# Kernel optimization log

Measured on AMD Instinct MI355X. Metric: run time of the kernel, lower is better.

## Reference

```python
import jax, jax.numpy as jnp
import numpy as np

B, L, C, P, H, DK, MRD = 16, 1024, 512, 64, 8, 64, 7
STD = 0.02


def _layernorm(x, g, b):
    mu = x.mean(-1, keepdims=True)
    var = ((x - mu) ** 2).mean(-1, keepdims=True)
    return (x - mu) / jnp.sqrt(var + 1e-5) * g + b


def _rel_pos_table(L, m):
    i = jnp.arange(L)
    d = jnp.abs(i[:, None] - i[None, :]).astype(jnp.float32)
    d = jnp.where(d > m, m + jnp.log2(jnp.maximum(d - m, 1.0)), d)
    return jnp.clip(d, 0, 2 * m).astype(jnp.int32)  # (L, L) in [0, 2m]


def setup_inputs() -> dict:
    key = jax.random.key(0)
    ks = jax.random.split(key, 16)
    inp = {
        'qx': jax.random.normal(ks[0], (B, L, C), jnp.float32),
        'kx': jax.random.normal(ks[1], (B, L, C), jnp.float32),
        'vx': jax.random.normal(ks[2], (B, L, C), jnp.float32),
        'maskPAD': jnp.ones((B, L, L), jnp.int32),
        'Wp': jax.random.normal(ks[3], (C, P)) * STD,
        'bp': jnp.zeros((P,)),
        'WQ': jax.random.normal(ks[4], (C, H * DK)) * STD,
        'bQ': jnp.zeros((H * DK,)),
        'WK': jax.random.normal(ks[5], (C, H * DK)) * STD,
        'bK': jnp.zeros((H * DK,)),
        'WV': jax.random.normal(ks[6], (C, H * DK)) * STD,
        'bV': jnp.zeros((H * DK,)),
        'WO': jax.random.normal(ks[7], (H * DK, C)) * STD,
        'bO': jnp.zeros((C,)),
        'embK': jax.random.normal(ks[8], (2 * MRD + 1, H)) * STD,
        'embB': jax.random.normal(ks[9], (2 * MRD + 1, H)) * STD,
        'ln1_g': jnp.ones((C,)), 'ln1_b': jnp.zeros((C,)),
        'ln2_g': jnp.ones((C,)), 'ln2_b': jnp.zeros((C,)),
        'W1': jax.random.normal(ks[10], (C, 4 * C)) * STD,
        'b1': jnp.zeros((4 * C,)),
        'W2': jax.random.normal(ks[11], (4 * C, C)) * STD,
        'b2': jnp.zeros((C,)),
    }
    return inp


def reference(qx, kx, vx, maskPAD, Wp, bp, WQ, bQ, WK, bK, WV, bV, WO, bO,
              embK, embB, ln1_g, ln1_b, ln2_g, ln2_b, W1, b1, W2, b2):
    B_, L_, C_ = qx.shape
    P_ = Wp.shape[1]
    H_ = embK.shape[1]
    DK_ = WV.shape[1] // H_
    m = (embK.shape[0] - 1) // 2

    # pseudo-token attention pooling
    pScore = vx @ Wp + bp                                   # (B, L, P)
    pad = (maskPAD[:, 0] == 0)                              # (B, L)
    pScore = jnp.where(pad[:, :, None], -2.0 ** 15, pScore)
    pAlpha = jax.nn.softmax(pScore, axis=1)                 # softmax over L
    kxp = jnp.einsum('blp,blc->bpc', pAlpha, kx)            # (B, P, C)
    vxp = jnp.einsum('blp,blc->bpc', pAlpha, vx)
    pA = jax.lax.stop_gradient(pAlpha)                      # .detach()

    # multi-head attention vs pseudo tokens
    q = (qx @ WQ + bQ).reshape(B_, L_, H_, DK_).transpose(0, 2, 1, 3)   # (B,H,L,dk)
    k = (kxp @ WK + bK).reshape(B_, P_, H_, DK_).transpose(0, 2, 1, 3)  # (B,H,P,dk)
    v = (vxp @ WV + bV).reshape(B_, P_, H_, DK_).transpose(0, 2, 1, 3)
    scores = jnp.einsum('bhld,bhpd->bhlp', q, k) / np.sqrt(DK_).astype(np.float32)

    # relative position multiplicative/additive bias, pooled through pA
    tab = _rel_pos_table(L_, m)                             # (L, L)
    Krel = embK[tab].transpose(2, 0, 1)                     # (H, L, L)
    brel = embB[tab].transpose(2, 0, 1)
    Kb = jnp.einsum('hlm,bmp->bhlp', Krel, pA)
    bb = jnp.einsum('hlm,bmp->bhlp', brel, pA)
    scores = scores * Kb + bb

    alpha = jax.nn.softmax(scores, axis=3)
    z = jnp.einsum('bhlp,bhpd->bhld', alpha, v)
    z = z.transpose(0, 2, 1, 3).reshape(B_, L_, H_ * DK_)
    z = z @ WO + bO

    # FFN block (residuals against vx, post-LN)
    z1 = _layernorm(vx + z, ln1_g, ln1_b)
    ffn = jax.nn.gelu(z1 @ W1 + b1, approximate=False) @ W2 + b2
    x = _layernorm(z1 + ffn, ln2_g, ln2_b)
    return x
```

## Files before the change

### kernel.cpp

```cpp
#include <hip/hip_runtime.h>
#include <hip/hip_bf16.h>

#define BI   16
#define LSEQ 1024
#define CDIM 512
#define PDIM 64
#define HH   8
#define DKK  64

typedef __hip_bfloat16 bf16;
typedef unsigned short u16;
typedef __attribute__((ext_vector_type(8))) short bf16x8;
typedef __attribute__((ext_vector_type(4))) float f32x4;

__constant__ int c_dlo[15] = {0,1,2,3,4,5,6,7, 9,11,15,23,39, 71,135};
__constant__ int c_dhi[15] = {0,1,2,3,4,5,6,8,10,14,22,38,70,134,1023};

__device__ __forceinline__ float b2f(u16 u) {
    union { unsigned int i; float f; } c; c.i = ((unsigned int)u) << 16; return c.f;
}
__device__ __forceinline__ u16 f2bu(float v) {
    bf16 h = __float2bfloat16(v);
    return *(u16*)&h;
}
__device__ __forceinline__ float ldDyn(const void* p, size_t i, int f) {
    return f ? ((const float*)p)[i] : b2f(((const u16*)p)[i]);
}
__device__ __forceinline__ void ld4Dyn(const void* p, size_t i, int f, float* o) {
    if (f) { float4 v = *(const float4*)((const float*)p + i);
             o[0]=v.x; o[1]=v.y; o[2]=v.z; o[3]=v.w; }
    else   { ushort4 u = *(const ushort4*)((const u16*)p + i);
             o[0]=b2f(u.x); o[1]=b2f(u.y); o[2]=b2f(u.z); o[3]=b2f(u.w); }
}

__device__ __forceinline__ void gll16(const u16* g, u16* l) {
    __builtin_amdgcn_global_load_lds(
        (const __attribute__((address_space(1))) unsigned int*)g,
        (__attribute__((address_space(3))) unsigned int*)l,
        16, 0, 0);
}

__device__ __forceinline__ float wsum(float v) {
    #pragma unroll
    for (int o = 32; o; o >>= 1) v += __shfl_xor(v, o, 64);
    return v;
}
__device__ __forceinline__ float wmax(float v) {
    #pragma unroll
    for (int o = 32; o; o >>= 1) v = fmaxf(v, __shfl_xor(v, o, 64));
    return v;
}

__global__ void k_detect(const unsigned int* __restrict__ qw, int* __restrict__ flag) {
    __shared__ int cnt;
    if (threadIdx.x == 0) cnt = 0;
    __syncthreads();
    int local = 0;
    for (int i = threadIdx.x; i < 4096; i += 256) {
        float fv = b2f((u16)(qw[i] & 0xFFFFu));
        float af = fabsf(fv);
        if (fv == 0.0f || (af >= 0.0009765625f && af <= 32.0f)) local++;
    }
    atomicAdd(&cnt, local);
    __syncthreads();
    if (threadIdx.x == 0) flag[0] = (cnt >= 2048) ? 0 : 1;
}

__global__ __launch_bounds__(256) void k_cvt2(
    const void* __restrict__ s0, u16* __restrict__ d0,
    const void* __restrict__ s1, u16* __restrict__ d1,
    const int* __restrict__ flag, int n)
{
    const int fA = flag[0];
    const void* src = blockIdx.y ? s1 : s0;
    u16* dst = blockIdx.y ? d1 : d0;
    int i = (blockIdx.x * 256 + threadIdx.x) * 4;
    if (i >= n) return;
    float t[4]; ld4Dyn(src, i, fA, t);
    ushort4 o; o.x = f2bu(t[0]); o.y = f2bu(t[1]); o.z = f2bu(t[2]); o.w = f2bu(t[3]);
    *(ushort4*)(dst + i) = o;
}

__device__ __forceinline__ void transp_core(
    const void* W, u16* WT, int fd, int Kd, int Nd, int bx, int by)
{
    __shared__ u16 t[32][33];
    const int tx = threadIdx.x & 31, ty = threadIdx.x >> 5;
    #pragma unroll
    for (int r = 0; r < 32; r += 8) {
        int k = by * 32 + ty + r, n = bx * 32 + tx;
        t[ty + r][tx] = f2bu(ldDyn(W, (size_t)k * Nd + n, fd));
    }
    __syncthreads();
    #pragma unroll
    for (int r = 0; r < 32; r += 8) {
        int n = bx * 32 + ty + r, k = by * 32 + tx;
        WT[(size_t)n * Kd + k] = t[tx][ty + r];
    }
}

__global__ __launch_bounds__(256) void k_transp(
    const void* __restrict__ W, u16* __restrict__ WT, const int* __restrict__ flag,
    int Kd, int Nd)
{
    transp_core(W, WT, flag[0], Kd, Nd, blockIdx.x, blockIdx.y);
}

__global__ __launch_bounds__(256) void k_transp4(
    const void* __restrict__ W0, u16* __restrict__ T0,
    const void* __restrict__ W1, u16* __restrict__ T1,
    const void* __restrict__ W2, u16* __restrict__ T2,
    const void* __restrict__ W3, u16* __restrict__ T3,
    const int* __restrict__ flag)
{
    const void* W; u16* T;
    switch (blockIdx.z) {
        case 0: W = W0; T = T0; break;
        case 1: W = W1; T = T1; break;
        case 2: W = W2; T = T2; break;
        default: W = W3; T = T3; break;
    }
    transp_core(W, T, flag[0], 512, 512, blockIdx.x, blockIdx.y);
}

__global__ __launch_bounds__(256) void k_transpcv(
    const void* __restrict__ kx, const u16* __restrict__ vxb,
    u16* __restrict__ kxT, u16* __restrict__ vxT, const int* __restrict__ flag)
{
    const int t = blockIdx.z >> 4;
    const int b = blockIdx.z & 15;
    const int l0 = blockIdx.x * 64, c0 = blockIdx.y * 32;
    __shared__ u16 s[32][72];
    const int tid = threadIdx.x;
    if (t == 0) {
        const int fd = flag[0];
        #pragma unroll
        for (int p = 0; p < 2; ++p) {
            int l = (tid >> 3) + p * 32, c4 = (tid & 7) * 4;
            float v[4];
            ld4Dyn(kx, ((size_t)b * LSEQ + l0 + l) * CDIM + c0 + c4, fd, v);
            #pragma unroll
            for (int k = 0; k < 4; ++k) s[c4 + k][l] = f2bu(v[k]);
        }
    } else {
        #pragma unroll
        for (int p = 0; p < 2; ++p) {
            int l = (tid >> 3) + p * 32, c4 = (tid & 7) * 4;
            ushort4 u = *(const ushort4*)&vxb[((size_t)b * LSEQ + l0 + l) * CDIM + c0 + c4];
            s[c4 + 0][l] = u.x; s[c4 + 1][l] = u.y;
            s[c4 + 2][l] = u.z; s[c4 + 3][l] = u.w;
        }
    }
    __syncthreads();
    u16* dst = t ? vxT : kxT;
    #pragma unroll
    for (int p = 0; p < 2; ++p) {
        int c = (tid >> 4) + p * 16, l4 = (tid & 15) * 4;
        *(ushort4*)&dst[((size_t)b * CDIM + c0 + c) * LSEQ + l0 + l4] =
            *(const ushort4*)&s[c][l4];
    }
}

__device__ __forceinline__ void gemm_core(
    u16 (*As)[32], u16 (*Bs)[32],
    const u16* A, const u16* BT, const void* bias, const u16* res, void* Cc, int fd,
    int K, int lda, int ldbt, int ldc, size_t bOff, int mode, int outBf, int perm,
    int m0, int n0)
{
    const int tid = threadIdx.x;
    const int wave = tid >> 6, lane = tid & 63;
    const int q = lane >> 4, l16 = lane & 15;
    const int wm = (wave >> 1) * 64, wn = (wave & 1) * 64;
    const int srow = wave * 16 + (lane >> 2);
    const int scol = ((lane & 3) ^ ((lane >> 3) & 3)) * 8;
    const int rchk = (l16 >> 1) & 3;
    const int nt = K >> 5;

    f32x4 acc[4][4];
    #pragma unroll
    for (int i = 0; i < 4; ++i)
        #pragma unroll
        for (int j = 0; j < 4; ++j) acc[i][j] = (f32x4){0.f, 0.f, 0.f, 0.f};

    auto stage = [&](int t, int buf) {
        const int o = buf * 128;
        #pragma unroll
        for (int pass = 0; pass < 2; ++pass) {
            int row = pass * 64 + srow;
            gll16(A + (size_t)(m0 + row) * lda + t * 32 + scol,
                  &As[o + pass * 64 + wave * 16][0]);
            gll16(BT + (size_t)(n0 + row) * ldbt + t * 32 + scol,
                  &Bs[o + pass * 64 + wave * 16][0]);
        }
    };

    stage(0, 0);

    for (int t = 0; t < nt; ++t) {
        if (t + 1 < nt) {
            stage(t + 1, (t + 1) & 1);
            asm volatile("s_waitcnt vmcnt(4)" ::: "memory");
        } else {
            asm volatile("s_waitcnt vmcnt(0)" ::: "memory");
        }
        __builtin_amdgcn_sched_barrier(0);
        __builtin_amdgcn_s_barrier();

        const int cb = (t & 1) * 128;
        bf16x8 af[4], bfr[4];
        #pragma unroll
        for (int i = 0; i < 4; ++i)
            af[i] = *(const bf16x8*)&As[cb + wm + i * 16 + l16][(q ^ rchk) * 8];
        #pragma unroll
        for (int j = 0; j < 4; ++j)
            bfr[j] = *(const bf16x8*)&Bs[cb + wn + j * 16 + l16][(q ^ rchk) * 8];
        #pragma unroll
        for (int i = 0; i < 4; ++i)
            #pragma unroll
            for (int j = 0; j < 4; ++j)
                acc[i][j] = __builtin_amdgcn_mfma_f32_16x16x32_bf16(af[i], bfr[j], acc[i][j], 0, 0, 0);

        if (t + 1 < nt) {
            asm volatile("s_waitcnt lgkmcnt(0)" ::: "memory");
            __builtin_amdgcn_sched_barrier(0);
            __builtin_amdgcn_s_barrier();
        }
    }

    #pragma unroll
    for (int i = 0; i < 4; ++i) {
        int row = m0 + wm + i * 16 + q * 4;
        #pragma unroll
        for (int j = 0; j < 4; ++j) {
            int col = n0 + wn + j * 16 + l16;
            #pragma unroll
            for (int r = 0; r < 4; ++r) {
                float v = acc[i][j][r];
                int m = row + r;
                if (mode == 2) {
                    v += ldDyn(bias, bOff + col, fd) + b2f(res[(size_t)m * ldc + col]);
                    ((float*)Cc)[(size_t)m * ldc + col] = v;
                } else {
                    v += ldDyn(bias, bOff + col, fd);
                    if (mode == 1) v = 0.5f * v * (1.0f + erff(v * 0.70710678118654752f));
                    size_t idx = perm ? (size_t)((m >> 6) << 15) + ((size_t)col << 6) + (m & 63)
                                      : (size_t)m * ldc + col;
                    if (outBf) ((u16*)Cc)[idx] = f2bu(v);
                    else       ((float*)Cc)[idx] = v;
                }
            }
        }
    }
}

__global__ __launch_bounds__(256) void gemm_mfma(
    const u16* __restrict__ A, const u16* __restrict__ BT, const void* __restrict__ bias,
    const u16* __restrict__ res, void* __restrict__ Cc, const int* __restrict__ flag,
    int K, int lda, int ldbt, int ldc, size_t bOff, int mode, int outBf, int perm)
{
    __shared__ u16 As[256][32];
    __shared__ u16 Bs[256][32];
    const int lin = blockIdx.y * gridDim.x + blockIdx.x;
    const int chunk = (gridDim.x * gridDim.y) >> 3;
    const int wg = (lin & 7) * chunk + (lin >> 3);
    const int bx = wg % gridDim.x, by = wg / gridDim.x;
    gemm_core(As, Bs, A, BT, bias, res, Cc, flag[0], K, lda, ldbt, ldc, bOff,
              mode, outBf, perm, by * 128, bx * 128);
}

__global__ __launch_bounds__(256) void gemm_kv(
    const u16* __restrict__ A0, const u16* __restrict__ A1,
    const u16* __restrict__ BT0, const u16* __restrict__ BT1,
    const void* __restrict__ b0, const void* __restrict__ b1,
    void* __restrict__ C0, void* __restrict__ C1, const int* __restrict__ flag)
{
    __shared__ u16 As[256][32];
    __shared__ u16 Bs[256][32];
    const int z = blockIdx.z;
    gemm_core(As, Bs, z ? A1 : A0, z ? BT1 : BT0, z ? b1 : b0, nullptr,
              z ? C1 : C0, flag[0],
              CDIM, CDIM, CDIM, CDIM, 0, 0, 1, z ? 1 : 0,
              blockIdx.y * 128, blockIdx.x * 128);
}

__global__ __launch_bounds__(256) void gemm_pool(
    const u16* __restrict__ pAT, const u16* __restrict__ kxT,
    const u16* __restrict__ vxT, u16* __restrict__ kvxb)
{
    __shared__ u16 As[128][32];
    __shared__ u16 Bs[256][32];
    const int b = blockIdx.y;
    const int n0 = blockIdx.x * 128;
    const u16* Ag = pAT + (size_t)b * (PDIM * LSEQ);
    const u16* Bg = (blockIdx.z ? vxT : kxT) + (size_t)b * (CDIM * LSEQ);
    u16* Cg = kvxb + (size_t)blockIdx.z * 524288 + (size_t)b * (PDIM * CDIM);

    const int tid = threadIdx.x;
    const int wave = tid >> 6, lane = tid & 63;
    const int q = lane >> 4, l16 = lane & 15;
    const int wm = (wave >> 1) * 32, wn = (wave & 1) * 64;
    const int srow = lane >> 2, scol = (lane & 3) * 8;

    f32x4 acc[2][4];
    #pragma unroll
    for (int i = 0; i < 2; ++i)
        #pragma unroll
        for (int j = 0; j < 4; ++j) acc[i][j] = (f32x4){0.f, 0.f, 0.f, 0.f};

    gll16(Ag + (size_t)(wave * 16 + srow) * LSEQ + scol, &As[wave * 16][0]);
    #pragma unroll
    for (int pass = 0; pass < 2; ++pass)
        gll16(Bg + (size_t)(n0 + wave * 32 + pass * 16 + srow) * LSEQ + scol,
              &Bs[wave * 32 + pass * 16][0]);
    __syncthreads();

    int cur = 0;
    for (int k0 = 0; k0 < LSEQ; k0 += 32) {
        if (k0 + 32 < LSEQ) {
            const int na = (cur ^ 1) * 64, nb = (cur ^ 1) * 128;
            gll16(Ag + (size_t)(wave * 16 + srow) * LSEQ + (k0 + 32) + scol,
                  &As[na + wave * 16][0]);
            #pragma unroll
            for (int pass = 0; pass < 2; ++pass)
                gll16(Bg + (size_t)(n0 + wave * 32 + pass * 16 + srow) * LSEQ + (k0 + 32) + scol,
                      &Bs[nb + wave * 32 + pass * 16][0]);
        }
        const int ca = cur * 64, cb = cur * 128;
        bf16x8 af[2], bfr[4];
        #pragma unroll
        for (int i = 0; i < 2; ++i) af[i] = *(const bf16x8*)&As[ca + wm + i * 16 + l16][q * 8];
        #pragma unroll
        for (int j = 0; j < 4; ++j) bfr[j] = *(const bf16x8*)&Bs[cb + wn + j * 16 + l16][q * 8];
        #pragma unroll
        for (int i = 0; i < 2; ++i)
            #pragma unroll
            for (int j = 0; j < 4; ++j)
                acc[i][j] = __builtin_amdgcn_mfma_f32_16x16x32_bf16(af[i], bfr[j], acc[i][j], 0, 0, 0);
        __syncthreads();
        cur ^= 1;
    }

    #pragma unroll
    for (int i = 0; i < 2; ++i) {
        int row = wm + i * 16 + q * 4;
        #pragma unroll
        for (int j = 0; j < 4; ++j) {
            int col = n0 + wn + j * 16 + l16;
            #pragma unroll
            for (int r = 0; r < 4; ++r)
                Cg[(size_t)(row + r) * CDIM + col] = f2bu(acc[i][j][r]);
        }
    }
}

__global__ __launch_bounds__(256) void gemm_mfma64(
    const u16* __restrict__ A, const u16* __restrict__ BT, const void* __restrict__ bias,
    float* __restrict__ Cc, const int* __restrict__ flag,
    int K, int lda, int ldbt)
{
    const int fd = flag[0];
    __shared__ u16 As[256][32];
    __shared__ u16 Bs[128][32];
    const int m0 = blockIdx.y * 128;
    const int tid = threadIdx.x;
    const int wave = tid >> 6, lane = tid & 63;
    const int q = lane >> 4, l16 = lane & 15;
    const int wm = wave * 32;
    const int srow = wave * 16 + (lane >> 2);
    const int scol = (lane & 3) * 8;

    f32x4 acc[2][4];
    #pragma unroll
    for (int i = 0; i < 2; ++i)
        #pragma unroll
        for (int j = 0; j < 4; ++j) acc[i][j] = (f32x4){0.f, 0.f, 0.f, 0.f};

    #pragma unroll
    for (int pass = 0; pass < 2; ++pass) {
        int row = pass * 64 + srow;
        gll16(A + (size_t)(m0 + row) * lda + scol, &As[pass * 64 + wave * 16][0]);
    }
    gll16(BT + (size_t)srow * ldbt + scol, &Bs[wave * 16][0]);
    __syncthreads();

    int cur = 0;
    for (int k0 = 0; k0 < K; k0 += 32) {
        if (k0 + 32 < K) {
            const int na = (cur ^ 1) * 128, nb = (cur ^ 1) * 64;
            #pragma unroll
            for (int pass = 0; pass < 2; ++pass) {
                int row = pass * 64 + srow;
                gll16(A + (size_t)(m0 + row) * lda + (k0 + 32) + scol,
                      &As[na + pass * 64 + wave * 16][0]);
            }
            gll16(BT + (size_t)srow * ldbt + (k0 + 32) + scol, &Bs[nb + wave * 16][0]);
        }
        const int ca = cur * 128, cb = cur * 64;
        bf16x8 af[2], bfr[4];
        #pragma unroll
        for (int i = 0; i < 2; ++i) af[i] = *(const bf16x8*)&As[ca + wm + i * 16 + l16][q * 8];
        #pragma unroll
        for (int j = 0; j < 4; ++j) bfr[j] = *(const bf16x8*)&Bs[cb + j * 16 + l16][q * 8];
        #pragma unroll
        for (int i = 0; i < 2; ++i)
            #pragma unroll
            for (int j = 0; j < 4; ++j)
                acc[i][j] = __builtin_amdgcn_mfma_f32_16x16x32_bf16(af[i], bfr[j], acc[i][j], 0, 0, 0);
        __syncthreads();
        cur ^= 1;
    }

    #pragma unroll
    for (int i = 0; i < 2; ++i) {
        int row = m0 + wm + i * 16 + q * 4;
        #pragma unroll
        for (int j = 0; j < 4; ++j) {
            int col = j * 16 + l16;
            #pragma unroll
            for (int r = 0; r < 4; ++r)
                Cc[(size_t)(row + r) * 64 + col] = acc[i][j][r] + ldDyn(bias, col, fd);
        }
    }
}

__global__ __launch_bounds__(256) void gemm_att(
    const u16* __restrict__ Abase, const u16* __restrict__ Bbase,
    void* __restrict__ outp, int mode)
{
    __shared__ u16 Aq[2][128][32];
    __shared__ u16 Bk[2][64][32];
    const int bh = blockIdx.y;
    const int b = bh >> 3, h = bh & 7;
    const int m0 = blockIdx.x * 128;
    const int tid = threadIdx.x;
    const int wave = tid >> 6, lane = tid & 63;
    const int q = lane >> 4, l16 = lane & 15;

    const u16* Ag; const u16* Bg; int lda, ldb;
    if (mode == 0) {
        Ag = Abase + ((size_t)b * LSEQ + m0) * CDIM + h * 64;  lda = CDIM;
        Bg = Bbase + (size_t)b * 32768 + h * 64;               ldb = CDIM;
    } else {
        Ag = Abase + ((size_t)bh * LSEQ + m0) * 64;            lda = 64;
        Bg = Bbase + (size_t)b * 32768 + (size_t)h * 64 * 64;  ldb = 64;
    }

    const int srow = lane >> 2;
    const int scol = (lane & 3) * 8;
    #pragma unroll
    for (int half = 0; half < 2; ++half) {
        #pragma unroll
        for (int pass = 0; pass < 2; ++pass) {
            int row = pass * 64 + wave * 16 + srow;
            gll16(Ag + (size_t)row * lda + half * 32 + scol,
                  &Aq[half][pass * 64 + wave * 16][0]);
        }
        gll16(Bg + (size_t)(wave * 16 + srow) * ldb + half * 32 + scol,
              &Bk[half][wave * 16][0]);
    }
    __syncthreads();

    f32x4 acc[2][4];
    #pragma unroll
    for (int i = 0; i < 2; ++i)
        #pragma unroll
        for (int j = 0; j < 4; ++j) acc[i][j] = (f32x4){0.f, 0.f, 0.f, 0.f};

    #pragma unroll
    for (int kk = 0; kk < 2; ++kk) {
        bf16x8 af[2], bfr[4];
        #pragma unroll
        for (int i = 0; i < 2; ++i)
            af[i] = *(const bf16x8*)&Aq[kk][wave * 32 + i * 16 + l16][q * 8];
        #pragma unroll
        for (int j = 0; j < 4; ++j)
            bfr[j] = *(const bf16x8*)&Bk[kk][j * 16 + l16][q * 8];
        #pragma unroll
        for (int i = 0; i < 2; ++i)
            #pragma unroll
            for (int j = 0; j < 4; ++j)
                acc[i][j] = __builtin_amdgcn_mfma_f32_16x16x32_bf16(af[i], bfr[j], acc[i][j], 0, 0, 0);
    }

    #pragma unroll
    for (int i = 0; i < 2; ++i) {
        int row = m0 + wave * 32 + i * 16 + q * 4;
        #pragma unroll
        for (int j = 0; j < 4; ++j) {
            int col = j * 16 + l16;
            #pragma unroll
            for (int r = 0; r < 4; ++r) {
                if (mode == 0) {
                    ((float*)outp)[((size_t)bh * LSEQ + row + r) * 64 + col] =
                        0.125f * acc[i][j][r];
                } else {
                    ((u16*)outp)[((size_t)b * LSEQ + row + r) * CDIM + h * 64 + col] =
                        f2bu(acc[i][j][r]);
                }
            }
        }
    }
}

__global__ __launch_bounds__(256) void k_softscan(
    const float* __restrict__ psc, const int* __restrict__ maskPAD,
    u16* __restrict__ pAT, float* __restrict__ cumT)
{
    const int b = blockIdx.x >> 6;
    const int p = blockIdx.x & 63;
    const int tid = threadIdx.x;
    __shared__ float s0[1024], s1[1024];
    __shared__ float redA[4], redB[4];

    float acc[4];
    #pragma unroll
    for (int r = 0; r < 4; ++r) {
        int m = tid + r * 256;
        float a = psc[((size_t)b * LSEQ + m) * PDIM + p];
        if (maskPAD[(size_t)b * LSEQ * LSEQ + m] == 0) a = -32768.0f;
        acc[r] = a;
    }
    float mx = fmaxf(fmaxf(acc[0], acc[1]), fmaxf(acc[2], acc[3]));
    mx = wmax(mx);
    if ((tid & 63) == 0) redA[tid >> 6] = mx;
    __syncthreads();
    mx = fmaxf(fmaxf(redA[0], redA[1]), fmaxf(redA[2], redA[3]));

    float e[4], ls = 0.f;
    #pragma unroll
    for (int r = 0; r < 4; ++r) { e[r] = expf(acc[r] - mx); ls += e[r]; }
    ls = wsum(ls);
    if ((tid & 63) == 0) redB[tid >> 6] = ls;
    __syncthreads();
    float inv = 1.0f / (redB[0] + redB[1] + redB[2] + redB[3]);

    #pragma unroll
    for (int r = 0; r < 4; ++r) {
        int m = tid + r * 256;
        float pa = e[r] * inv;
        pAT[((size_t)b * PDIM + p) * LSEQ + m] = f2bu(pa);
        s0[m] = pa;
    }
    __syncthreads();

    float* src = s0; float* dst = s1;
    for (int off = 1; off < 1024; off <<= 1) {
        #pragma unroll
        for (int r = 0; r < 4; ++r) {
            int i = tid + r * 256;
            float v = src[i];
            if (i >= off) v += src[i - off];
            dst[i] = v;
        }
        __syncthreads();
        float* t = src; src = dst; dst = t;
    }
    size_t cb = (size_t)b * (LSEQ + 1) * PDIM + p;
    if (tid == 0) cumT[cb] = 0.f;
    #pragma unroll
    for (int r = 0; r < 4; ++r) {
        int i = tid + r * 256;
        cumT[cb + (size_t)(i + 1) * PDIM] = src[i];
    }
}

__global__ __launch_bounds__(512) void k_sm(
    const float* __restrict__ raw, u16* __restrict__ alb,
    const float* __restrict__ cumT,
    const void* __restrict__ embK, const void* __restrict__ embB,
    const int* __restrict__ flag)
{
    const int fd = flag[0];
    const int b = blockIdx.x >> 10;
    const int l = blockIdx.x & 1023;
    const int tid = threadIdx.x;
    __shared__ float S[15][PDIM];
    __shared__ float eK[120], eB[120];

    if (tid < 120) { eK[tid] = ldDyn(embK, tid, fd); eB[tid] = ldDyn(embB, tid, fd); }

    const float* cb = cumT + (size_t)b * (LSEQ + 1) * PDIM;
    for (int idx = tid; idx < 960; idx += 512) {
        int t = idx >> 6, pp = idx & 63;
        float s;
        if (t == 0) {
            s = cb[(size_t)(l + 1) * 64 + pp] - cb[(size_t)l * 64 + pp];
        } else {
            s = 0.f;
            int hi = l - c_dlo[t];
            int lo = l - c_dhi[t]; if (lo < 0) lo = 0;
            if (hi >= lo) s += cb[(size_t)(hi + 1) * 64 + pp] - cb[(size_t)lo * 64 + pp];
            lo = l + c_dlo[t];
            hi = l + c_dhi[t]; if (hi > 1023) hi = 1023;
            if (lo <= hi) s += cb[(size_t)(hi + 1) * 64 + pp] - cb[(size_t)lo * 64 + pp];
        }
        S[t][pp] = s;
    }
    __syncthreads();

    const int h = tid >> 6, p = tid & 63;
    float kbm = 0.f, bbm = 0.f;
    #pragma unroll
    for (int t = 0; t < 15; ++t) {
        float sv = S[t][p];
        kbm += eK[t * 8 + h] * sv;
        bbm += eB[t * 8 + h] * sv;
    }
    size_t idx = (((size_t)b * 8 + h) * LSEQ + l) * 64 + p;
    float sc = raw[idx] * kbm + bbm;
    float mx = wmax(sc);
    float e  = expf(sc - mx);
    float ssum = wsum(e);
    alb[idx] = f2bu(e / ssum);
}

__global__ __launch_bounds__(512) void k_ln(
    const void* __restrict__ a, const u16* __restrict__ badd,
    const void* __restrict__ g, const void* __restrict__ be, const int* __restrict__ flag,
    void* __restrict__ out, float* __restrict__ out2, const void* __restrict__ bias2,
    int aKind, int outKind)
{
    const int fd = flag[0];
    const int fA = (aKind == 2) ? fd : aKind;
    const int fO = (outKind == 2) ? fd : outKind;
    const size_t row = blockIdx.x;
    const int c = threadIdx.x;
    float x = ldDyn(a, row * CDIM + c, fA);
    if (badd) x += b2f(badd[row * CDIM + c]);

    __shared__ float rA[8], rB[8];
    float s = wsum(x);
    if ((c & 63) == 0) rA[c >> 6] = s;
    __syncthreads();
    float tot = 0.f;
    #pragma unroll
    for (int w = 0; w < 8; ++w) tot += rA[w];
    float mu = tot * (1.0f / 512.0f);
    float dv = x - mu;
    float s2 = wsum(dv * dv);
    if ((c & 63) == 0) rB[c >> 6] = s2;
    __syncthreads();
    float v2 = 0.f;
    #pragma unroll
    for (int w = 0; w < 8; ++w) v2 += rB[w];
    float y = dv * rsqrtf(v2 * (1.0f / 512.0f) + 1e-5f) * ldDyn(g, c, fd) + ldDyn(be, c, fd);
    if (fO) ((float*)out)[row * CDIM + c] = y;
    else    ((u16*)out)[row * CDIM + c] = f2bu(y);
    if (out2) out2[row * CDIM + c] = y + ldDyn(bias2, c, fd);
}

extern "C" void kernel_launch(void* const* d_in, const int* in_sizes, int n_in,
                              void* d_out, int out_size, void* d_ws, size_t ws_size,
                              hipStream_t stream)
{
    (void)in_sizes; (void)n_in; (void)out_size; (void)ws_size;
    const void* qx   = d_in[0];
    const void* kx   = d_in[1];
    const void* vx   = d_in[2];
    const int*  mask = (const int*)d_in[3];
    const void* Wp   = d_in[4];
    const void* bp   = d_in[5];
    const void* WQ   = d_in[6];
    const void* bQ   = d_in[7];
    const void* WK   = d_in[8];
    const void* bK   = d_in[9];
    const void* WV   = d_in[10];
    const void* bV   = d_in[11];
    const void* WO   = d_in[12];
    const void* bO   = d_in[13];
    const void* embK = d_in[14];
    const void* embB = d_in[15];
    const void* l1g  = d_in[16];
    const void* l1b  = d_in[17];
    const void* l2g  = d_in[18];
    const void* l2b  = d_in[19];
    const void* W1   = d_in[20];
    const void* b1   = d_in[21];
    const void* W2   = d_in[22];
    const void* b2   = d_in[23];

    float* ws     = (float*)d_ws;
    int*   flag   = (int*)d_ws;
    float* outF   = ws + 64;
    float* psc    = ws + 64;
    float* cumT   = ws + 1048640;
    u16*   pAT    = (u16*)(ws + 2098240);
    u16*   kbh    = (u16*)(ws + 2622528);
    u16*   vbT    = (u16*)(ws + 2884672);
    u16*   albuf  = (u16*)(ws + 3146816);
    u16*   kvxb   = (u16*)(ws + 7341120);
    u16*   qz     = (u16*)(ws + 8388672);
    u16*   hidden = (u16*)(ws + 12582976);
    u16*   qxb    = hidden;
    u16*   zo     = qxb;
    u16*   vxb    = (u16*)(ws + 16777280);
    u16*   kxT    = (u16*)(ws + 20971584);
    u16*   vxT    = (u16*)(ws + 25165888);
    float* rawbuf = ws + 20971584;
    u16*   WqT    = (u16*)(ws + 29360192);
    u16*   WkT    = (u16*)(ws + 29491264);
    u16*   WvT    = (u16*)(ws + 29622336);
    u16*   WoT    = (u16*)(ws + 29753408);
    u16*   W1T    = (u16*)(ws + 29884480);
    u16*   W2T    = (u16*)(ws + 30408768);
    u16*   WpT    = (u16*)(ws + 30933056);

    const int MROW = BI * LSEQ;

    k_detect<<<dim3(1), dim3(256), 0, stream>>>((const unsigned int*)qx, flag);
    k_cvt2<<<dim3(MROW * CDIM / 1024, 2), dim3(256), 0, stream>>>(
        qx, qxb, vx, vxb, flag, MROW * CDIM);
    k_transp4<<<dim3(16, 16, 4), dim3(256), 0, stream>>>(
        WQ, WqT, WK, WkT, WV, WvT, WO, WoT, flag);
    k_transp<<<dim3(2, 16),  dim3(256), 0, stream>>>(Wp, WpT, flag, 512, 64);
    k_transp<<<dim3(64, 16), dim3(256), 0, stream>>>(W1, W1T, flag, 512, 2048);
    k_transp<<<dim3(16, 64), dim3(256), 0, stream>>>(W2, W2T, flag, 2048, 512);
    k_transpcv<<<dim3(16, 16, 32), dim3(256), 0, stream>>>(kx, vxb, kxT, vxT, flag);

    gemm_mfma64<<<dim3(1, MROW / 128), dim3(256), 0, stream>>>(
        vxb, WpT, bp, psc, flag, CDIM, CDIM, CDIM);
    k_softscan<<<dim3(BI * PDIM), dim3(256), 0, stream>>>(psc, mask, pAT, cumT);
    gemm_pool<<<dim3(4, 16, 2), dim3(256), 0, stream>>>(pAT, kxT, vxT, kvxb);
    gemm_mfma<<<dim3(4, MROW / 128), dim3(256), 0, stream>>>(
        qxb, WqT, bQ, nullptr, qz, flag, CDIM, CDIM, CDIM, CDIM, 0, 0, 1, 0);
    gemm_kv<<<dim3(4, 8, 2), dim3(256), 0, stream>>>(
        kvxb, kvxb + 524288, WkT, WvT, bK, bV, kbh, vbT, flag);
    gemm_att<<<dim3(8, BI * HH), dim3(256), 0, stream>>>(qz, kbh, rawbuf, 0);
    k_sm<<<dim3(BI * LSEQ), dim3(512), 0, stream>>>(
        rawbuf, albuf, cumT, embK, embB, flag);
    gemm_att<<<dim3(8, BI * HH), dim3(256), 0, stream>>>(albuf, vbT, qz, 1);
    gemm_mfma<<<dim3(4, MROW / 128), dim3(256), 0, stream>>>(
        qz, WoT, bO, nullptr, zo, flag, CDIM, CDIM, CDIM, CDIM, 0, 0, 1, 0);
    k_ln<<<dim3(MROW), dim3(512), 0, stream>>>(
        vx, zo, l1g, l1b, flag, qz, nullptr, nullptr, 2, 0);
    gemm_mfma<<<dim3(16, MROW / 128), dim3(256), 0, stream>>>(
        qz, W1T, b1, nullptr, hidden, flag, CDIM, CDIM, CDIM, 2048, 0, 1, 1, 0);
    gemm_mfma<<<dim3(4, MROW / 128), dim3(256), 0, stream>>>(
        hidden, W2T, b2, qz, outF, flag, 2048, 2048, 2048, CDIM, 0, 2, 0, 0);
    k_ln<<<dim3(MROW), dim3(512), 0, stream>>>(
        outF, nullptr, l2g, l2b, flag, d_out, nullptr, nullptr, 1, 2);
}
```

Measured before the change: 642.0 us.

## Widen GEMM tiles to 128x256 with 8 waves, fast GELU, bf16 FFN output

The shared GEMM core now uses 512 threads (8 waves) computing 128x256 tiles, so each A tile is reused across twice as many columns and the grid halves. The bias loads are hoisted out of the epilogue loop. The exact erff in GELU is replaced by an Abramowitz-Stegun polynomial with a fast exp and reciprocal. The second FFN GEMM now writes bf16 instead of fp32 before the final layernorm, which cuts write and read traffic. The cost is more LDS and registers per block, lower occupancy, and some added precision error from the approximate GELU and the bf16 intermediate.

```diff
diff --git a/kernel.cpp b/kernel.cpp
--- a/kernel.cpp
+++ b/kernel.cpp
@@ -49,6 +49,18 @@
     #pragma unroll
     for (int o = 32; o; o >>= 1) v = fmaxf(v, __shfl_xor(v, o, 64));
     return v;
+}
+
+__device__ __forceinline__ float gelu_f(float v) {
+    float x  = v * 0.70710678118654752f;
+    float ax = fabsf(x);
+    float t  = __builtin_amdgcn_rcpf(1.0f + 0.3275911f * ax);
+    float p  = t * (0.254829592f + t * (-0.284496736f + t * (1.421413741f +
+               t * (-1.453152027f + t * 1.061405429f))));
+    float e  = __expf(-ax * ax);
+    float er = 1.0f - p * e;
+    er = (x < 0.0f) ? -er : er;
+    return 0.5f * v * (1.0f + er);
 }
 
 __global__ void k_detect(const unsigned int* __restrict__ qw, int* __restrict__ flag) {
@@ -170,8 +182,8 @@
     const int tid = threadIdx.x;
     const int wave = tid >> 6, lane = tid & 63;
     const int q = lane >> 4, l16 = lane & 15;
-    const int wm = (wave >> 1) * 64, wn = (wave & 1) * 64;
-    const int srow = wave * 16 + (lane >> 2);
+    const int wm = (wave >> 2) * 64, wn = (wave & 3) * 64;
+    const int srow = lane >> 2;
     const int scol = ((lane & 3) ^ ((lane >> 3) & 3)) * 8;
     const int rchk = (l16 >> 1) & 3;
     const int nt = K >> 5;
@@ -183,15 +195,12 @@
         for (int j = 0; j < 4; ++j) acc[i][j] = (f32x4){0.f, 0.f, 0.f, 0.f};
 
     auto stage = [&](int t, int buf) {
-        const int o = buf * 128;
-        #pragma unroll
-        for (int pass = 0; pass < 2; ++pass) {
-            int row = pass * 64 + srow;
-            gll16(A + (size_t)(m0 + row) * lda + t * 32 + scol,
-                  &As[o + pass * 64 + wave * 16][0]);
-            gll16(BT + (size_t)(n0 + row) * ldbt + t * 32 + scol,
-                  &Bs[o + pass * 64 + wave * 16][0]);
-        }
+        gll16(A + (size_t)(m0 + wave * 16 + srow) * lda + t * 32 + scol,
+              &As[buf * 128 + wave * 16][0]);
+        #pragma unroll
+        for (int pass = 0; pass < 2; ++pass)
+            gll16(BT + (size_t)(n0 + pass * 128 + wave * 16 + srow) * ldbt + t * 32 + scol,
+                  &Bs[buf * 256 + pass * 128 + wave * 16][0]);
     };
 
     stage(0, 0);
@@ -199,21 +208,21 @@
     for (int t = 0; t < nt; ++t) {
         if (t + 1 < nt) {
             stage(t + 1, (t + 1) & 1);
-            asm volatile("s_waitcnt vmcnt(4)" ::: "memory");
+            asm volatile("s_waitcnt vmcnt(3)" ::: "memory");
         } else {
             asm volatile("s_waitcnt vmcnt(0)" ::: "memory");
         }
         __builtin_amdgcn_sched_barrier(0);
         __builtin_amdgcn_s_barrier();
 
-        const int cb = (t & 1) * 128;
+        const int ca = (t & 1) * 128, cbB = (t & 1) * 256;
         bf16x8 af[4], bfr[4];
         #pragma unroll
         for (int i = 0; i < 4; ++i)
-            af[i] = *(const bf16x8*)&As[cb + wm + i * 16 + l16][(q ^ rchk) * 8];
+            af[i] = *(const bf16x8*)&As[ca + wm + i * 16 + l16][(q ^ rchk) * 8];
         #pragma unroll
         for (int j = 0; j < 4; ++j)
-            bfr[j] = *(const bf16x8*)&Bs[cb + wn + j * 16 + l16][(q ^ rchk) * 8];
+            bfr[j] = *(const bf16x8*)&Bs[cbB + wn + j * 16 + l16][(q ^ rchk) * 8];
         #pragma unroll
         for (int i = 0; i < 4; ++i)
             #pragma unroll
@@ -227,6 +236,11 @@
         }
     }
 
+    float bv[4];
+    #pragma unroll
+    for (int j = 0; j < 4; ++j)
+        bv[j] = ldDyn(bias, bOff + (size_t)(n0 + wn + j * 16 + l16), fd);
+
     #pragma unroll
     for (int i = 0; i < 4; ++i) {
         int row = m0 + wm + i * 16 + q * 4;
@@ -235,14 +249,14 @@
             int col = n0 + wn + j * 16 + l16;
             #pragma unroll
             for (int r = 0; r < 4; ++r) {
-                float v = acc[i][j][r];
+                float v = acc[i][j][r] + bv[j];
                 int m = row + r;
                 if (mode == 2) {
-                    v += ldDyn(bias, bOff + col, fd) + b2f(res[(size_t)m * ldc + col]);
-                    ((float*)Cc)[(size_t)m * ldc + col] = v;
+                    v += b2f(res[(size_t)m * ldc + col]);
+                    if (outBf) ((u16*)Cc)[(size_t)m * ldc + col] = f2bu(v);
+                    else       ((float*)Cc)[(size_t)m * ldc + col] = v;
                 } else {
-                    v += ldDyn(bias, bOff + col, fd);
-                    if (mode == 1) v = 0.5f * v * (1.0f + erff(v * 0.70710678118654752f));
+                    if (mode == 1) v = gelu_f(v);
                     size_t idx = perm ? (size_t)((m >> 6) << 15) + ((size_t)col << 6) + (m & 63)
                                       : (size_t)m * ldc + col;
                     if (outBf) ((u16*)Cc)[idx] = f2bu(v);
@@ -253,34 +267,34 @@
     }
 }
 
-__global__ __launch_bounds__(256) void gemm_mfma(
+__global__ __launch_bounds__(512) void gemm_mfma(
     const u16* __restrict__ A, const u16* __restrict__ BT, const void* __restrict__ bias,
     const u16* __restrict__ res, void* __restrict__ Cc, const int* __restrict__ flag,
     int K, int lda, int ldbt, int ldc, size_t bOff, int mode, int outBf, int perm)
 {
     __shared__ u16 As[256][32];
-    __shared__ u16 Bs[256][32];
+    __shared__ u16 Bs[512][32];
     const int lin = blockIdx.y * gridDim.x + blockIdx.x;
     const int chunk = (gridDim.x * gridDim.y) >> 3;
     const int wg = (lin & 7) * chunk + (lin >> 3);
     const int bx = wg % gridDim.x, by = wg / gridDim.x;
     gemm_core(As, Bs, A, BT, bias, res, Cc, flag[0], K, lda, ldbt, ldc, bOff,
-              mode, outBf, perm, by * 128, bx * 128);
-}
-
-__global__ __launch_bounds__(256) void gemm_kv(
+              mode, outBf, perm, by * 128, bx * 256);
+}
+
+__global__ __launch_bounds__(512) void gemm_kv(
     const u16* __restrict__ A0, const u16* __restrict__ A1,
     const u16* __restrict__ BT0, const u16* __restrict__ BT1,
     const void* __restrict__ b0, const void* __restrict__ b1,
     void* __restrict__ C0, void* __restrict__ C1, const int* __restrict__ flag)
 {
     __shared__ u16 As[256][32];
-    __shared__ u16 Bs[256][32];
+    __shared__ u16 Bs[512][32];
     const int z = blockIdx.z;
     gemm_core(As, Bs, z ? A1 : A0, z ? BT1 : BT0, z ? b1 : b0, nullptr,
               z ? C1 : C0, flag[0],
               CDIM, CDIM, CDIM, CDIM, 0, 0, 1, z ? 1 : 0,
-              blockIdx.y * 128, blockIdx.x * 128);
+              blockIdx.y * 128, blockIdx.x * 256);
 }
 
 __global__ __launch_bounds__(256) void gemm_pool(
@@ -681,7 +695,7 @@
 
     float* ws     = (float*)d_ws;
     int*   flag   = (int*)d_ws;
-    float* outF   = ws + 64;
+    u16*   outFb  = (u16*)(ws + 64);
     float* psc    = ws + 64;
     float* cumT   = ws + 1048640;
     u16*   pAT    = (u16*)(ws + 2098240);
@@ -721,22 +735,22 @@
         vxb, WpT, bp, psc, flag, CDIM, CDIM, CDIM);
     k_softscan<<<dim3(BI * PDIM), dim3(256), 0, stream>>>(psc, mask, pAT, cumT);
     gemm_pool<<<dim3(4, 16, 2), dim3(256), 0, stream>>>(pAT, kxT, vxT, kvxb);
-    gemm_mfma<<<dim3(4, MROW / 128), dim3(256), 0, stream>>>(
+    gemm_mfma<<<dim3(2, MROW / 128), dim3(512), 0, stream>>>(
         qxb, WqT, bQ, nullptr, qz, flag, CDIM, CDIM, CDIM, CDIM, 0, 0, 1, 0);
-    gemm_kv<<<dim3(4, 8, 2), dim3(256), 0, stream>>>(
+    gemm_kv<<<dim3(2, 8, 2), dim3(512), 0, stream>>>(
         kvxb, kvxb + 524288, WkT, WvT, bK, bV, kbh, vbT, flag);
     gemm_att<<<dim3(8, BI * HH), dim3(256), 0, stream>>>(qz, kbh, rawbuf, 0);
     k_sm<<<dim3(BI * LSEQ), dim3(512), 0, stream>>>(
         rawbuf, albuf, cumT, embK, embB, flag);
     gemm_att<<<dim3(8, BI * HH), dim3(256), 0, stream>>>(albuf, vbT, qz, 1);
-    gemm_mfma<<<dim3(4, MROW / 128), dim3(256), 0, stream>>>(
+    gemm_mfma<<<dim3(2, MROW / 128), dim3(512), 0, stream>>>(
         qz, WoT, bO, nullptr, zo, flag, CDIM, CDIM, CDIM, CDIM, 0, 0, 1, 0);
     k_ln<<<dim3(MROW), dim3(512), 0, stream>>>(
         vx, zo, l1g, l1b, flag, qz, nullptr, nullptr, 2, 0);
-    gemm_mfma<<<dim3(16, MROW / 128), dim3(256), 0, stream>>>(
+    gemm_mfma<<<dim3(8, MROW / 128), dim3(512), 0, stream>>>(
         qz, W1T, b1, nullptr, hidden, flag, CDIM, CDIM, CDIM, 2048, 0, 1, 1, 0);
-    gemm_mfma<<<dim3(4, MROW / 128), dim3(256), 0, stream>>>(
-        hidden, W2T, b2, qz, outF, flag, 2048, 2048, 2048, CDIM, 0, 2, 0, 0);
+    gemm_mfma<<<dim3(2, MROW / 128), dim3(512), 0, stream>>>(
+        hidden, W2T, b2, qz, outFb, flag, 2048, 2048, 2048, CDIM, 0, 2, 1, 0);
     k_ln<<<dim3(MROW), dim3(512), 0, stream>>>(
-        outF, nullptr, l2g, l2b, flag, d_out, nullptr, nullptr, 1, 2);
-}
+        outFb, nullptr, l2g, l2b, flag, d_out, nullptr, nullptr, 0, 2);
+}
```

After: 613.2 us. -4.5%, faster.
